# Performance work log

Measured on AMD Instinct MI355X. Metric: run time of the kernel, lower is better.

## Reference

```python
import jax, jax.numpy as jnp
import numpy as np

B = 4096          # fused tokens (batch)
E = 1024          # attnConfig embed_size == MoE emb_size
OUT = E // 4      # per-branch feature dim (self.output)
N_EXP = 8         # number of experts
TOP = 2           # top-k routing
H = 8             # attention heads
HD = E // H       # head dim
HID = 4 * E       # expert MLP hidden
IMG = 64 * 64     # flattened single-channel image
W_IMP = 0.01      # importance loss weight


def setup_inputs() -> dict:
    key = jax.random.key(0)
    ks = jax.random.split(key, 24)
    n = lambda i, shp, sc=1.0: jax.random.normal(ks[i], shp, jnp.float32) * sc
    inp = {
        'source': n(0, (B, 1, 64, 64)),
        'target': n(1, (B, 1, 64, 64)),
        'background': n(2, (B, 1, 64, 64)),
        'image': n(3, (B, E)),
        'text': n(4, (B, E)),
        # shared encoder (stub: flatten -> fc to OUT, shared across s/t/b)
        'W_enc': n(5, (IMG, OUT), 0.02), 'b_enc': jnp.zeros((OUT,), jnp.float32),
        # linerImg
        'W_img': n(6, (E, OUT), 0.02), 'b_img': jnp.zeros((OUT,), jnp.float32),
        # cross attention
        'Wq': n(7, (E, E), 0.02), 'bq': jnp.zeros((E,), jnp.float32),
        'Wk': n(8, (E, E), 0.02), 'bk': jnp.zeros((E,), jnp.float32),
        'Wv': n(9, (E, E), 0.02), 'bv': jnp.zeros((E,), jnp.float32),
        'Wo': n(10, (E, E), 0.02), 'bo': jnp.zeros((E,), jnp.float32),
        # gate
        'W_gate': n(11, (E, N_EXP), 0.02), 'b_gate': jnp.zeros((N_EXP,), jnp.float32),
        # experts: per-expert 2-layer MLP E->HID->E
        'W1': n(12, (N_EXP, E, HID), 0.02), 'b1': jnp.zeros((N_EXP, HID), jnp.float32),
        'W2': n(13, (N_EXP, HID, E), 0.02), 'b2': jnp.zeros((N_EXP, E), jnp.float32),
    }
    return inp


def reference(source, target, background, image, text,
              W_enc, b_enc, W_img, b_img,
              Wq, bq, Wk, bk, Wv, bv, Wo, bo,
              W_gate, b_gate, W1, b1, W2, b2):
    enc = lambda a: a.reshape(a.shape[0], -1) @ W_enc + b_enc      # shared_encoder stub
    s = enc(source); t = enc(target); bg = enc(background)        # [B, OUT] each
    img = jax.nn.silu(image @ W_img + b_img)                      # [B, OUT]
    x = jnp.concatenate([s, t, bg, img], axis=1)                  # [B, E] visionFeatures

    # cross attention with seq_len 1 for both x (query) and text (key/value)
    q = (x @ Wq + bq).reshape(B, H, HD)
    k = (text @ Wk + bk).reshape(B, H, HD)
    v = (text @ Wv + bv).reshape(B, H, HD)
    scores = jnp.sum(q * k, axis=-1, keepdims=True) / jnp.sqrt(jnp.float32(HD))  # [B,H,1]
    attw = jax.nn.softmax(scores[..., None], axis=-1)[..., 0]     # softmax over 1 key == 1
    att = (attw * v).reshape(B, E) @ Wo + bo                       # [B, E]

    gate_logits = att @ W_gate + b_gate                            # [B, N_EXP]
    gate_prob = jax.nn.softmax(gate_logits, axis=-1)               # eval mode: no noise
    top_w, top_idx = jax.lax.top_k(gate_prob, TOP)                 # [B, TOP]
    top_w = jax.nn.softmax(top_w, axis=-1)                         # renormalize over top-k

    # dense-dispatch equivalent of the per-expert gather/index_add loop
    h = jax.nn.gelu(jnp.einsum('be,neh->nbh', x, W1) + b1[:, None, :])   # [N,B,HID]
    y_all = jnp.einsum('nbh,nhe->nbe', h, W2) + b2[:, None, :]           # [N,B,E]
    combine = jnp.zeros((B, N_EXP), jnp.float32).at[
        jnp.arange(B)[:, None], top_idx].add(top_w)                      # [B,N]
    y = jnp.einsum('nbe,bn->be', y_all, combine)                          # [B,E]

    importance = gate_prob.sum(axis=0)                             # [N_EXP]
    importance_loss = W_IMP * (jnp.std(importance, ddof=1) / jnp.mean(importance)) ** 2
    return (y, gate_prob, importance_loss)
```

## Files before the change

### kernel.cpp

```cpp
#include <hip/hip_runtime.h>
#include <hip/hip_bf16.h>
#include <stdint.h>

typedef __bf16 bf16_t;
typedef bf16_t bf16x8 __attribute__((ext_vector_type(8)));
typedef float f32x4 __attribute__((ext_vector_type(4)));
typedef uint16_t u16x8 __attribute__((ext_vector_type(8)));

static constexpr int B_TOK  = 4096;
static constexpr int E_DIM  = 1024;
static constexpr int N_EXPC = 8;
static constexpr int HID    = 4096;
static constexpr int IMGSZ  = 4096;
static constexpr int NSLOT  = 2 * B_TOK;
static constexpr int NTIL   = 71;

#define DEVI __device__ __forceinline__

DEVI int imin(int a, int b) { return a < b ? a : b; }

DEVI uint16_t f2bf(float f) {
  union { float f; uint32_t u; } v; v.f = f;
  uint32_t u = v.u;
  return (uint16_t)((u + 0x7FFFu + ((u >> 16) & 1u)) >> 16);
}

DEVI float bf2f(uint16_t u) {
  union { uint32_t i; float f; } v; v.i = (uint32_t)u << 16; return v.f;
}

DEVI void gload_lds16(const void* g, void* l) {
  __builtin_amdgcn_global_load_lds((const __attribute__((address_space(1))) void*)g,
                                   (__attribute__((address_space(3))) void*)l, 16, 0, 0);
}

template<int N> DEVI void waitv() {
  if constexpr (N == 0)       asm volatile("s_waitcnt vmcnt(0)" ::: "memory");
  else if constexpr (N == 4)  asm volatile("s_waitcnt vmcnt(4)" ::: "memory");
  else if constexpr (N == 8)  asm volatile("s_waitcnt vmcnt(8)" ::: "memory");
  else if constexpr (N == 10) asm volatile("s_waitcnt vmcnt(10)" ::: "memory");
}

#define BAR() do { __builtin_amdgcn_sched_barrier(0); __builtin_amdgcn_s_barrier(); \
                   __builtin_amdgcn_sched_barrier(0); } while (0)

#define MFMA16(a, b, c) __builtin_amdgcn_mfma_f32_16x16x32_bf16((a), (b), (c), 0, 0, 0)

DEVI void transW_body(int bid, const float* W1, const float* W2,
                      const float* We, const float* Wi,
                      uint16_t* W1T, uint16_t* W2T, uint16_t* WeT, uint16_t* WiT,
                      float (*tile)[65])
{
  const float* in; uint16_t* out; int R, C, c0, r0;
  if (bid < 8192) {
    int e = bid >> 10, rem = bid & 1023;
    R = 1024; C = 4096;
    c0 = (rem & 63) * 64; r0 = (rem >> 6) * 64;
    in = W1 + (size_t)e * R * C; out = W1T + (size_t)e * R * C;
  } else if (bid < 16384) {
    int i = bid - 8192; int e = i >> 10, rem = i & 1023;
    R = 4096; C = 1024;
    c0 = (rem & 15) * 64; r0 = (rem >> 4) * 64;
    in = W2 + (size_t)e * R * C; out = W2T + (size_t)e * R * C;
  } else if (bid < 16640) {
    int i = bid - 16384;
    R = 4096; C = 256;
    c0 = (i & 3) * 64; r0 = (i >> 2) * 64;
    in = We; out = WeT;
  } else {
    int i = bid - 16640;
    R = 1024; C = 256;
    c0 = (i & 3) * 64; r0 = (i >> 2) * 64;
    in = Wi; out = WiT;
  }
  int t = threadIdx.x;
  #pragma unroll
  for (int i = 0; i < 4; ++i) {
    int rr = i * 16 + (t >> 4), c4 = (t & 15) * 4;
    f32x4 v = *(const f32x4*)&in[(size_t)(r0 + rr) * C + c0 + c4];
    tile[rr][c4 + 0] = v[0]; tile[rr][c4 + 1] = v[1];
    tile[rr][c4 + 2] = v[2]; tile[rr][c4 + 3] = v[3];
  }
  __syncthreads();
  #pragma unroll
  for (int i = 0; i < 2; ++i) {
    int c = i * 32 + (t >> 3), j = t & 7;
    u16x8 o;
    #pragma unroll
    for (int k = 0; k < 8; ++k) o[k] = f2bf(tile[j * 8 + k][c]);
    *(u16x8*)&out[(size_t)(c0 + c) * R + r0 + j * 8] = o;
  }
}

DEVI void matf_body(int kblk, const float* W, const float* G, float* out)
{
  int k = kblk * 4 + (threadIdx.x >> 6);
  int lane = threadIdx.x & 63;
  float a0 = 0.f, a1 = 0.f, a2 = 0.f, a3 = 0.f, a4 = 0.f, a5 = 0.f, a6 = 0.f, a7 = 0.f;
  for (int m = lane; m < E_DIM; m += 64) {
    float w = W[(size_t)k * E_DIM + m];
    const float* gm = &G[m * 8];
    a0 = __builtin_fmaf(w, gm[0], a0); a1 = __builtin_fmaf(w, gm[1], a1);
    a2 = __builtin_fmaf(w, gm[2], a2); a3 = __builtin_fmaf(w, gm[3], a3);
    a4 = __builtin_fmaf(w, gm[4], a4); a5 = __builtin_fmaf(w, gm[5], a5);
    a6 = __builtin_fmaf(w, gm[6], a6); a7 = __builtin_fmaf(w, gm[7], a7);
  }
  #pragma unroll
  for (int off = 32; off; off >>= 1) {
    a0 += __shfl_xor(a0, off); a1 += __shfl_xor(a1, off);
    a2 += __shfl_xor(a2, off); a3 += __shfl_xor(a3, off);
    a4 += __shfl_xor(a4, off); a5 += __shfl_xor(a5, off);
    a6 += __shfl_xor(a6, off); a7 += __shfl_xor(a7, off);
  }
  if (lane == 0) {
    float* o = &out[k * 8];
    o[0] = a0; o[1] = a1; o[2] = a2; o[3] = a3;
    o[4] = a4; o[5] = a5; o[6] = a6; o[7] = a7;
  }
}

__global__ __launch_bounds__(256)
void prep1_k(const float* __restrict__ W1, const float* __restrict__ W2,
             const float* __restrict__ We, const float* __restrict__ Wi,
             uint16_t* __restrict__ W1T, uint16_t* __restrict__ W2T,
             uint16_t* __restrict__ WeT, uint16_t* __restrict__ WiT,
             const float* __restrict__ Wo, const float* __restrict__ Wg,
             float* __restrict__ g1c,
             const float* __restrict__ bv, float* __restrict__ part,
             int* __restrict__ counts)
{
  __shared__ float tile[64][65];
  int bid = blockIdx.x;
  if (bid < 16704) {
    transW_body(bid, W1, W2, We, Wi, W1T, W2T, WeT, WiT, tile);
  } else if (bid < 16960) {
    matf_body(bid - 16704, Wo, Wg, g1c);
  } else if (bid < 16968) {
    int b = bid - 16960, t = threadIdx.x;
    f32x4 acc = {0.f, 0.f, 0.f, 0.f};
    for (int k = b * 128; k < b * 128 + 128; ++k) {
      float s = bv[k];
      f32x4 w = *(const f32x4*)&Wo[(size_t)k * E_DIM + t * 4];
      acc[0] = __builtin_fmaf(s, w[0], acc[0]);
      acc[1] = __builtin_fmaf(s, w[1], acc[1]);
      acc[2] = __builtin_fmaf(s, w[2], acc[2]);
      acc[3] = __builtin_fmaf(s, w[3], acc[3]);
    }
    *(f32x4*)&part[(size_t)b * E_DIM + t * 4] = acc;
  } else {
    if (threadIdx.x < 8) counts[threadIdx.x] = 0;
  }
}

__global__ __launch_bounds__(256)
void prep2_k(const float* __restrict__ Wv, const float* __restrict__ g1c,
             float* __restrict__ G3,
             const float* __restrict__ part, const float* __restrict__ bo,
             const float* __restrict__ Wg, const float* __restrict__ bg,
             float* __restrict__ gb)
{
  int bid = blockIdx.x;
  if (bid < 256) {
    matf_body(bid, Wv, g1c, G3);
  } else {
    __shared__ float t1s[E_DIM];
    int t = threadIdx.x;
    for (int j = t; j < E_DIM; j += 256) {
      float s = bo[j];
      #pragma unroll
      for (int b = 0; b < 8; ++b) s += part[(size_t)b * E_DIM + j];
      t1s[j] = s;
    }
    __syncthreads();
    int wave = t >> 6, lane = t & 63;
    #pragma unroll
    for (int ei = 0; ei < 2; ++ei) {
      int e = wave * 2 + ei;
      float s = 0.f;
      for (int m = lane; m < E_DIM; m += 64) s = __builtin_fmaf(t1s[m], Wg[m * 8 + e], s);
      #pragma unroll
      for (int off = 32; off; off >>= 1) s += __shfl_xor(s, off);
      if (lane == 0) gb[e] = s + bg[e];
    }
  }
}

__global__ __launch_bounds__(256)
void gate_k(const float* __restrict__ text, const float* __restrict__ G3,
            const float* __restrict__ gb, float* __restrict__ gate_out,
            int* __restrict__ topIdx, float* __restrict__ topW,
            int* __restrict__ counts)
{
  __shared__ __align__(16) float sT[E_DIM];
  __shared__ float lg[8];
  int b = blockIdx.x, t = threadIdx.x;
  *(f32x4*)&sT[t * 4] = *(const f32x4*)&text[(size_t)b * E_DIM + t * 4];
  __syncthreads();
  int wave = t >> 6, lane = t & 63;
  #pragma unroll
  for (int ei = 0; ei < 2; ++ei) {
    int e = wave * 2 + ei;
    float s = 0.f;
    for (int k = lane; k < E_DIM; k += 64) s = __builtin_fmaf(sT[k], G3[k * 8 + e], s);
    #pragma unroll
    for (int off = 32; off; off >>= 1) s += __shfl_down(s, off);
    if (lane == 0) lg[e] = s + gb[e];
  }
  __syncthreads();
  if (t == 0) {
    float p[8];
    float mx = lg[0];
    for (int i = 1; i < 8; i++) mx = fmaxf(mx, lg[i]);
    float den = 0.f;
    for (int i = 0; i < 8; i++) { p[i] = __expf(lg[i] - mx); den += p[i]; }
    float inv = 1.f / den;
    for (int i = 0; i < 8; i++) { p[i] *= inv; gate_out[(size_t)b * 8 + i] = p[i]; }
    int i1 = 0;
    for (int i = 1; i < 8; i++) if (p[i] > p[i1]) i1 = i;
    int i2 = (i1 == 0) ? 1 : 0;
    for (int i = 0; i < 8; i++) if (i != i1 && p[i] > p[i2]) i2 = i;
    float ex = __expf(p[i2] - p[i1]);
    float w1 = 1.f / (1.f + ex), w2 = ex / (1.f + ex);
    topIdx[b * 2] = i1; topIdx[b * 2 + 1] = i2;
    topW[b * 2] = w1;  topW[b * 2 + 1] = w2;
    atomicAdd(&counts[i1], 1);
    atomicAdd(&counts[i2], 1);
  }
}

template<int BN, int EPI, bool GATHER, int NT>
__global__ __launch_bounds__(256, 3)
void gemm_p(const uint16_t* __restrict__ Ab, int lda,
            const uint16_t* __restrict__ BT, void* __restrict__ Cv, int ldc,
            const float* __restrict__ bias, int K,
            const int* __restrict__ meta, const int* __restrict__ perm,
            size_t bStride, int biasStride)
{
  constexpr int HN = BN / 2, FN = BN / 32;
  constexpr int OPS = (BN == 128 ? 4 : 3);
  constexpr int TOTAL = NTIL * NT, Q = TOTAL / 8, FULLB = 64 * NT;
  int bid = blockIdx.x;
  int wg = (bid & 7) * Q + (bid >> 3);
  int mtile, nt;
  if (wg < FULLB) { int rem = wg % (8 * NT); mtile = (wg / (8 * NT)) * 8 + (rem & 7); nt = rem >> 3; }
  else            { int rem = wg - FULLB;    mtile = 64 + rem % 7;                    nt = rem / 7; }
  if (mtile >= meta[0]) return;
  int e = meta[1 + 3 * mtile], rowBase = meta[2 + 3 * mtile], rows = meta[3 + 3 * mtile];
  const uint16_t* Bt = BT + (size_t)e * bStride;
  const float* bi = bias + (size_t)e * (size_t)biasStride;

  constexpr int ABUF = 8192;
  constexpr int BBUF = (BN == 128) ? 8192 : 4096;
  __shared__ __align__(16) char sAraw[3 * ABUF];
  __shared__ __align__(16) char sBraw[3 * BBUF];

  int t = threadIdx.x, wave = t >> 6, lane = t & 63;
  int wr = wave >> 1, wc = wave & 1;

  int rB = t >> 2;
  int slB = ((t & 3) ^ (rB & 3)) * 8;
  const uint16_t* gB0 = Bt + (size_t)(nt * BN + rB) * K + slB;
  const uint16_t* gB1 = Bt + (size_t)(nt * BN + rB + 64) * K + slB;

  int r0 = t >> 2, r1 = r0 + 64;
  int sl = ((t & 3) ^ (r0 & 3)) * 8;
  int rr0 = imin(r0, rows - 1), rr1 = imin(r1, rows - 1);
  int car0 = GATHER ? perm[rowBase + rr0] : rowBase + rr0;
  int car1 = GATHER ? perm[rowBase + rr1] : rowBase + rr1;
  const uint16_t* gA0 = Ab + (size_t)car0 * lda + sl;
  const uint16_t* gA1 = Ab + (size_t)car1 * lda + sl;

  char* laW = sAraw + wave * 1024;
  char* lbW = sBraw + wave * 1024;
  auto STAGE = [&](int kt, int c) {
    int ko = kt << 5;
    char* la = laW + c * ABUF;
    char* lb = lbW + c * BBUF;
    gload_lds16(gA0 + ko, la);
    gload_lds16(gA1 + ko, la + 4096);
    gload_lds16(gB0 + ko, lb);
    if constexpr (BN == 128) gload_lds16(gB1 + ko, lb + 4096);
  };

  f32x4 acc[4][FN];
  #pragma unroll
  for (int m = 0; m < 4; m++)
    #pragma unroll
    for (int n = 0; n < FN; n++)
      acc[m][n] = f32x4{0.f, 0.f, 0.f, 0.f};

  STAGE(0, 0);
  STAGE(1, 1);

  int fr = lane & 15;
  int rdoff = ((lane >> 4) ^ (lane & 3)) * 16;
  int c0 = 0, c2 = 2;
  int nk = K >> 5;

  for (int kt = 0; kt < nk; ++kt) {
    if (kt + 2 < nk) { STAGE(kt + 2, c2); waitv<2 * OPS>(); }
    else if (kt + 1 < nk) waitv<OPS>();
    else waitv<0>();
    BAR();

    const char* bA = sAraw + c0 * ABUF;
    const char* bB = sBraw + c0 * BBUF;
    bf16x8 af[4], bfr[FN];
    #pragma unroll
    for (int m = 0; m < 4; m++)
      af[m] = *(const bf16x8*)(bA + (wr * 64 + m * 16 + fr) * 64 + rdoff);
    #pragma unroll
    for (int n = 0; n < FN; n++)
      bfr[n] = *(const bf16x8*)(bB + (wc * HN + n * 16 + fr) * 64 + rdoff);
    #pragma unroll
    for (int m = 0; m < 4; m++)
      #pragma unroll
      for (int n = 0; n < FN; n++)
        acc[m][n] = MFMA16(af[m], bfr[n], acc[m][n]);

    BAR();
    c0 = (c0 == 2) ? 0 : c0 + 1;
    c2 = (c2 == 2) ? 0 : c2 + 1;
  }

  #pragma unroll
  for (int m = 0; m < 4; m++) {
    int lrow = wr * 64 + m * 16 + (lane >> 4) * 4;
    #pragma unroll
    for (int n = 0; n < FN; n++) {
      int col = nt * BN + wc * HN + n * 16 + (lane & 15);
      float bval = bi[col];
      #pragma unroll
      for (int r = 0; r < 4; r++) {
        int lr = lrow + r;
        if (lr >= rows) continue;
        float v = acc[m][n][r] + bval;
        size_t cr = (size_t)(rowBase + lr) * ldc + col;
        if (EPI == 3) {
          float u = v + 0.044715f * v * v * v;
          v = v / (1.f + __expf(-1.5957691216057308f * u));
          ((uint16_t*)Cv)[cr] = f2bf(v);
        } else if (EPI == 1) {
          ((uint16_t*)Cv)[cr] = f2bf(v);
        } else {
          ((float*)Cv)[cr] = v;
        }
      }
    }
  }
}

__global__ __launch_bounds__(256, 3)
void gemm_encR(const float* __restrict__ F0, const float* __restrict__ F1,
               const float* __restrict__ F2, const float* __restrict__ Fimg,
               const uint16_t* __restrict__ BTe, const uint16_t* __restrict__ BTi,
               float* __restrict__ Penc, float* __restrict__ Pimg)
{
  int z = blockIdx.z;
  const float* Af; const uint16_t* BT; float* P; int K, Kc, k0;
  if (z < 6) {
    int br = z >> 1, kc = z & 1;
    Af = (br == 0) ? F0 : (br == 1) ? F1 : F2;
    BT = BTe; P = Penc + (size_t)z * B_TOK * 256;
    K = IMGSZ; Kc = IMGSZ / 2; k0 = kc * Kc;
  } else {
    Af = Fimg; BT = BTi; P = Pimg;
    K = E_DIM; Kc = E_DIM; k0 = 0;
  }
  int rowBase = blockIdx.x * 64, nt = blockIdx.y;

  __shared__ __align__(16) char sB[3 * 8192];
  int t = threadIdx.x, wave = t >> 6, lane = t & 63;
  int fr = lane & 15, q4 = lane >> 4;

  const float* gA = Af + (size_t)(rowBase + wave * 16 + fr) * K + k0 + q4 * 8;

  int rloc = t >> 2;
  int ssw = ((t & 3) ^ (rloc & 3)) * 8;
  const uint16_t* gB0 = BT + (size_t)(nt * 128 + rloc) * K + k0 + ssw;
  const uint16_t* gB1 = gB0 + (size_t)64 * K;

  auto STB = [&](int kt, int c) {
    gload_lds16(gB0 + kt * 32, sB + c * 8192 + wave * 1024);
    gload_lds16(gB1 + kt * 32, sB + c * 8192 + 4096 + wave * 1024);
  };

  f32x4 acc[8];
  #pragma unroll
  for (int n = 0; n < 8; ++n) acc[n] = f32x4{0.f, 0.f, 0.f, 0.f};

  int nk = Kc >> 5;
  STB(0, 0); STB(1, 1);
  f32x4 aE0 = *(const f32x4*)(gA),      aE1 = *(const f32x4*)(gA + 4);
  f32x4 aO0 = *(const f32x4*)(gA + 32), aO1 = *(const f32x4*)(gA + 36);
  int c0 = 0, c2 = 2;
  int bRow = (q4 ^ (fr & 3)) * 16;

  auto step = [&](int kt, f32x4& aX0, f32x4& aX1) {
    bool m2 = kt + 2 < nk;
    if (m2) STB(kt + 2, c2);
    bf16x8 a;
    a[0] = (bf16_t)aX0[0]; a[1] = (bf16_t)aX0[1]; a[2] = (bf16_t)aX0[2]; a[3] = (bf16_t)aX0[3];
    a[4] = (bf16_t)aX1[0]; a[5] = (bf16_t)aX1[1]; a[6] = (bf16_t)aX1[2]; a[7] = (bf16_t)aX1[3];
    int kp = m2 ? kt + 2 : kt;
    aX0 = *(const f32x4*)(gA + kp * 32);
    aX1 = *(const f32x4*)(gA + kp * 32 + 4);
    if (m2) waitv<10>(); else waitv<0>();
    BAR();
    const char* bb = sB + c0 * 8192;
    bf16x8 bfr[8];
    #pragma unroll
    for (int n = 0; n < 8; ++n)
      bfr[n] = *(const bf16x8*)(bb + n * 1024 + fr * 64 + bRow);
    #pragma unroll
    for (int n = 0; n < 8; ++n) acc[n] = MFMA16(a, bfr[n], acc[n]);
    BAR();
    c0 = (c0 == 2) ? 0 : c0 + 1;
    c2 = (c2 == 2) ? 0 : c2 + 1;
  };

  for (int kt = 0; kt < nk; kt += 2) {
    step(kt, aE0, aE1);
    step(kt + 1, aO0, aO1);
  }

  #pragma unroll
  for (int n = 0; n < 8; ++n) {
    int col = nt * 128 + n * 16 + fr;
    #pragma unroll
    for (int r = 0; r < 4; ++r) {
      int row = rowBase + wave * 16 + q4 * 4 + r;
      P[(size_t)row * 256 + col] = acc[n][r];
    }
  }
}

__global__ __launch_bounds__(256)
void redupost_k(const float* __restrict__ Penc, const float* __restrict__ Pimg,
                const float* __restrict__ bEnc, const float* __restrict__ bImg,
                uint16_t* __restrict__ xb,
                const float* __restrict__ gate_out, float* __restrict__ out_loss,
                const int* __restrict__ counts, const int* __restrict__ topIdx,
                const float* __restrict__ topW,
                int* __restrict__ meta, int* __restrict__ perm,
                int* __restrict__ slotOf)
{
  int y = blockIdx.y, t = threadIdx.x;
  if (y < 4) {
    int row = blockIdx.x * 4 + (t >> 6);
    int c4 = (t & 63) * 4;
    bool img = (y == 3);
    const float* bias = img ? bImg : bEnc;
    f32x4 s = *(const f32x4*)&bias[c4];
    if (img) {
      s += *(const f32x4*)&Pimg[(size_t)row * 256 + c4];
      #pragma unroll
      for (int j = 0; j < 4; ++j) s[j] = s[j] / (1.f + __expf(-s[j]));
    } else {
      const float* p = Penc + (size_t)y * 2 * B_TOK * 256 + (size_t)row * 256 + c4;
      s += *(const f32x4*)p;
      s += *(const f32x4*)(p + (size_t)B_TOK * 256);
    }
    ushort4 o;
    o.x = f2bf(s[0]); o.y = f2bf(s[1]); o.z = f2bf(s[2]); o.w = f2bf(s[3]);
    *(ushort4*)&xb[(size_t)row * E_DIM + y * 256 + c4] = o;
    return;
  }
  if (blockIdx.x == 0) {
    float s[8] = {0.f, 0.f, 0.f, 0.f, 0.f, 0.f, 0.f, 0.f};
    for (int b = t; b < B_TOK; b += 256) {
      const float* g = &gate_out[(size_t)b * 8];
      #pragma unroll
      for (int e = 0; e < 8; ++e) s[e] += g[e];
    }
    __shared__ float red[8][256];
    #pragma unroll
    for (int e = 0; e < 8; ++e) red[e][t] = s[e];
    __syncthreads();
    for (int off = 128; off; off >>= 1) {
      if (t < off)
        #pragma unroll
        for (int e = 0; e < 8; ++e) red[e][t] += red[e][t + off];
      __syncthreads();
    }
    if (t == 0) {
      float m = 0.f;
      for (int e = 0; e < 8; e++) m += red[e][0];
      m *= 0.125f;
      float v = 0.f;
      for (int e = 0; e < 8; e++) { float d = red[e][0] - m; v += d * d; }
      v /= 7.f;
      out_loss[0] = 0.01f * v / (m * m);
    }
  } else if (blockIdx.x == 1) {
    __shared__ int sBases[8];
    __shared__ int sCursor[8];
    if (t == 0) {
      int a = 0, nt = 0;
      for (int e = 0; e < 8; e++) {
        sBases[e] = a; sCursor[e] = 0;
        int c = counts[e];
        for (int j = 0; j < c; j += 128) {
          meta[1 + 3 * nt] = e;
          meta[2 + 3 * nt] = a + j;
          meta[3 + 3 * nt] = (c - j < 128) ? (c - j) : 128;
          nt++;
        }
        a += c;
      }
      meta[0] = nt;
    }
    __syncthreads();
    for (int b = t; b < B_TOK; b += 256) {
      #pragma unroll
      for (int j = 0; j < 2; j++) {
        int e = topIdx[b * 2 + j];
        int pos = atomicAdd(&sCursor[e], 1);
        int slot = sBases[e] + pos;
        perm[slot] = b;
        slotOf[b * 2 + j] = slot;
      }
    }
  }
}

__global__ __launch_bounds__(256)
void combine_k(const uint16_t* __restrict__ Yg, const int* __restrict__ slotOf,
               const float* __restrict__ topW, float* __restrict__ y)
{
  int b = blockIdx.x, t = threadIdx.x;
  int s0 = slotOf[b * 2], s1 = slotOf[b * 2 + 1];
  float w0 = topW[b * 2], w1 = topW[b * 2 + 1];
  ushort4 ua = *(const ushort4*)&Yg[(size_t)s0 * E_DIM + t * 4];
  ushort4 uc = *(const ushort4*)&Yg[(size_t)s1 * E_DIM + t * 4];
  f32x4 r;
  r[0] = bf2f(ua.x) * w0 + bf2f(uc.x) * w1;
  r[1] = bf2f(ua.y) * w0 + bf2f(uc.y) * w1;
  r[2] = bf2f(ua.z) * w0 + bf2f(uc.z) * w1;
  r[3] = bf2f(ua.w) * w0 + bf2f(uc.w) * w1;
  *(f32x4*)&y[(size_t)b * E_DIM + t * 4] = r;
}

extern "C" void kernel_launch(void* const* d_in, const int* in_sizes, int n_in,
                              void* d_out, int out_size, void* d_ws, size_t ws_size,
                              hipStream_t stream)
{
  (void)in_sizes; (void)n_in; (void)out_size;
  const float* src   = (const float*)d_in[0];
  const float* tgt   = (const float*)d_in[1];
  const float* bgr   = (const float*)d_in[2];
  const float* image = (const float*)d_in[3];
  const float* text  = (const float*)d_in[4];
  const float* W_enc = (const float*)d_in[5];
  const float* b_enc = (const float*)d_in[6];
  const float* W_img = (const float*)d_in[7];
  const float* b_img = (const float*)d_in[8];
  const float* Wv    = (const float*)d_in[13];
  const float* bv    = (const float*)d_in[14];
  const float* Wo    = (const float*)d_in[15];
  const float* bo    = (const float*)d_in[16];
  const float* Wg    = (const float*)d_in[17];
  const float* bgg   = (const float*)d_in[18];
  const float* W1    = (const float*)d_in[19];
  const float* b1    = (const float*)d_in[20];
  const float* W2    = (const float*)d_in[21];
  const float* b2    = (const float*)d_in[22];

  float* out_y    = (float*)d_out;
  float* out_gate = out_y + (size_t)B_TOK * E_DIM;
  float* out_loss = out_gate + (size_t)B_TOK * N_EXPC;

  char* p = (char*)d_ws;
  auto alloc = [&](size_t bytes) { char* r = p; p += (bytes + 255) & ~(size_t)255; return r; };
  uint16_t* WencT = (uint16_t*)alloc((size_t)256 * IMGSZ * 2);
  uint16_t* WimgT = (uint16_t*)alloc((size_t)256 * E_DIM * 2);
  uint16_t* W1T   = (uint16_t*)alloc((size_t)N_EXPC * HID * E_DIM * 2);
  uint16_t* W2T   = (uint16_t*)alloc((size_t)N_EXPC * E_DIM * HID * 2);
  float* part  = (float*)alloc((size_t)8 * E_DIM * 4);
  float* g1c   = (float*)alloc((size_t)E_DIM * 8 * 4);
  float* G3    = (float*)alloc((size_t)E_DIM * 8 * 4);
  float* gbv   = (float*)alloc(64 * 4);
  int*   topIdx = (int*)alloc(B_TOK * 2 * 4);
  float* topW   = (float*)alloc(B_TOK * 2 * 4);
  int*   slotOf = (int*)alloc(B_TOK * 2 * 4);
  int*   counts = (int*)alloc(64 * 4);
  int*   meta   = (int*)alloc((1 + 3 * (NTIL + 1)) * 4 + 64);
  int*   perm   = (int*)alloc(NSLOT * 4);
  uint16_t* xbf  = (uint16_t*)alloc((size_t)B_TOK * E_DIM * 2);
  uint16_t* Hbuf = (uint16_t*)alloc((size_t)NSLOT * HID * 2);
  char* uni = alloc((size_t)7 * B_TOK * 256 * 4);
  float* Penc = (float*)uni;
  float* Pimg = Penc + (size_t)6 * B_TOK * 256;
  uint16_t* Yg = (uint16_t*)uni;
  if ((size_t)(p - (char*)d_ws) > ws_size) return;

  prep1_k<<<dim3(16969), 256, 0, stream>>>(W1, W2, W_enc, W_img, W1T, W2T, WencT, WimgT,
                                           Wo, Wg, g1c, bv, part, counts);
  prep2_k<<<dim3(257), 256, 0, stream>>>(Wv, g1c, G3, part, bo, Wg, bgg, gbv);
  gate_k<<<B_TOK, 256, 0, stream>>>(text, G3, gbv, out_gate, topIdx, topW, counts);
  gemm_encR<<<dim3(B_TOK / 64, 2, 7), 256, 0, stream>>>(
      src, tgt, bgr, image, WencT, WimgT, Penc, Pimg);
  redupost_k<<<dim3(B_TOK / 4, 5), 256, 0, stream>>>(
      Penc, Pimg, b_enc, b_img, xbf,
      out_gate, out_loss, counts, topIdx, topW, meta, perm, slotOf);

  gemm_p<128, 3, true, HID / 128><<<dim3(NTIL * (HID / 128)), 256, 0, stream>>>(
      xbf, E_DIM, W1T, Hbuf, HID, b1, E_DIM, meta, perm, (size_t)HID * E_DIM, HID);
  gemm_p<128, 1, false, E_DIM / 128><<<dim3(NTIL * (E_DIM / 128)), 256, 0, stream>>>(
      Hbuf, HID, W2T, Yg, E_DIM, b2, HID, meta, perm, (size_t)E_DIM * HID, E_DIM);

  combine_k<<<B_TOK, 256, 0, stream>>>(Yg, slotOf, topW, out_y);
}
```

Baseline: 633.9 us.

## Deepen GEMM K-step to 64 with double buffering and 8-way LDS swizzle

The grouped expert GEMM kernel now stages 64-wide K slices instead of 32-wide, using two LDS buffers of 16 KB each for A and B instead of a triple-buffered 32-wide ring. The LDS swizzle changes from 4-way to an 8-way XOR pattern over 128-byte rows. Each iteration issues twice as many MFMAs per barrier pair, which halves the barrier and wait overhead per unit of work. In exchange the pipeline is only one stage ahead, and the larger LDS footprint lowers occupancy (launch bounds drop from 3 to 2 blocks per CU).

```diff
diff --git a/kernel.cpp b/kernel.cpp
--- a/kernel.cpp
+++ b/kernel.cpp
@@ -36,7 +36,6 @@
 
 template<int N> DEVI void waitv() {
   if constexpr (N == 0)       asm volatile("s_waitcnt vmcnt(0)" ::: "memory");
-  else if constexpr (N == 4)  asm volatile("s_waitcnt vmcnt(4)" ::: "memory");
   else if constexpr (N == 8)  asm volatile("s_waitcnt vmcnt(8)" ::: "memory");
   else if constexpr (N == 10) asm volatile("s_waitcnt vmcnt(10)" ::: "memory");
 }
@@ -228,16 +227,14 @@
   }
 }
 
-template<int BN, int EPI, bool GATHER, int NT>
-__global__ __launch_bounds__(256, 3)
-void gemm_p(const uint16_t* __restrict__ Ab, int lda,
-            const uint16_t* __restrict__ BT, void* __restrict__ Cv, int ldc,
-            const float* __restrict__ bias, int K,
-            const int* __restrict__ meta, const int* __restrict__ perm,
-            size_t bStride, int biasStride)
-{
-  constexpr int HN = BN / 2, FN = BN / 32;
-  constexpr int OPS = (BN == 128 ? 4 : 3);
+template<int EPI, bool GATHER, int NT>
+__global__ __launch_bounds__(256, 2)
+void gemm_p64(const uint16_t* __restrict__ Ab, int lda,
+              const uint16_t* __restrict__ BT, void* __restrict__ Cv, int ldc,
+              const float* __restrict__ bias, int K,
+              const int* __restrict__ meta, const int* __restrict__ perm,
+              size_t bStride, int biasStride)
+{
   constexpr int TOTAL = NTIL * NT, Q = TOTAL / 8, FULLB = 64 * NT;
   int bid = blockIdx.x;
   int wg = (bid & 7) * Q + (bid >> 3);
@@ -249,86 +246,86 @@
   const uint16_t* Bt = BT + (size_t)e * bStride;
   const float* bi = bias + (size_t)e * (size_t)biasStride;
 
-  constexpr int ABUF = 8192;
-  constexpr int BBUF = (BN == 128) ? 8192 : 4096;
-  __shared__ __align__(16) char sAraw[3 * ABUF];
-  __shared__ __align__(16) char sBraw[3 * BBUF];
+  __shared__ __align__(16) char sA[2 * 16384];
+  __shared__ __align__(16) char sB[2 * 16384];
 
   int t = threadIdx.x, wave = t >> 6, lane = t & 63;
   int wr = wave >> 1, wc = wave & 1;
 
-  int rB = t >> 2;
-  int slB = ((t & 3) ^ (rB & 3)) * 8;
-  const uint16_t* gB0 = Bt + (size_t)(nt * BN + rB) * K + slB;
-  const uint16_t* gB1 = Bt + (size_t)(nt * BN + rB + 64) * K + slB;
-
-  int r0 = t >> 2, r1 = r0 + 64;
-  int sl = ((t & 3) ^ (r0 & 3)) * 8;
-  int rr0 = imin(r0, rows - 1), rr1 = imin(r1, rows - 1);
-  int car0 = GATHER ? perm[rowBase + rr0] : rowBase + rr0;
-  int car1 = GATHER ? perm[rowBase + rr1] : rowBase + rr1;
-  const uint16_t* gA0 = Ab + (size_t)car0 * lda + sl;
-  const uint16_t* gA1 = Ab + (size_t)car1 * lda + sl;
-
-  char* laW = sAraw + wave * 1024;
-  char* lbW = sBraw + wave * 1024;
+  int r8 = t >> 3;
+  int sg = (((t & 7) ^ (r8 & 7))) * 8;
+  const uint16_t* gA[4];
+  const uint16_t* gB[4];
+  #pragma unroll
+  for (int i = 0; i < 4; ++i) {
+    int ar = imin(i * 32 + r8, rows - 1);
+    int car = GATHER ? perm[rowBase + ar] : rowBase + ar;
+    gA[i] = Ab + (size_t)car * lda + sg;
+    gB[i] = Bt + (size_t)(nt * 128 + i * 32 + r8) * K + sg;
+  }
+  int wO = wave * 1024;
+
   auto STAGE = [&](int kt, int c) {
-    int ko = kt << 5;
-    char* la = laW + c * ABUF;
-    char* lb = lbW + c * BBUF;
-    gload_lds16(gA0 + ko, la);
-    gload_lds16(gA1 + ko, la + 4096);
-    gload_lds16(gB0 + ko, lb);
-    if constexpr (BN == 128) gload_lds16(gB1 + ko, lb + 4096);
+    int ko = kt << 6;
+    char* la = sA + c * 16384 + wO;
+    char* lb = sB + c * 16384 + wO;
+    #pragma unroll
+    for (int i = 0; i < 4; ++i) gload_lds16(gA[i] + ko, la + i * 4096);
+    #pragma unroll
+    for (int i = 0; i < 4; ++i) gload_lds16(gB[i] + ko, lb + i * 4096);
   };
 
-  f32x4 acc[4][FN];
+  f32x4 acc[4][4];
   #pragma unroll
   for (int m = 0; m < 4; m++)
     #pragma unroll
-    for (int n = 0; n < FN; n++)
+    for (int n = 0; n < 4; n++)
       acc[m][n] = f32x4{0.f, 0.f, 0.f, 0.f};
 
   STAGE(0, 0);
-  STAGE(1, 1);
-
-  int fr = lane & 15;
-  int rdoff = ((lane >> 4) ^ (lane & 3)) * 16;
-  int c0 = 0, c2 = 2;
-  int nk = K >> 5;
+
+  int fr = lane & 15, q4 = lane >> 4;
+  int nk = K >> 6;
 
   for (int kt = 0; kt < nk; ++kt) {
-    if (kt + 2 < nk) { STAGE(kt + 2, c2); waitv<2 * OPS>(); }
-    else if (kt + 1 < nk) waitv<OPS>();
+    int b = kt & 1, nb = b ^ 1;
+    bool more = kt + 1 < nk;
+    if (more) { STAGE(kt + 1, nb); waitv<8>(); }
     else waitv<0>();
     BAR();
 
-    const char* bA = sAraw + c0 * ABUF;
-    const char* bB = sBraw + c0 * BBUF;
-    bf16x8 af[4], bfr[FN];
-    #pragma unroll
-    for (int m = 0; m < 4; m++)
-      af[m] = *(const bf16x8*)(bA + (wr * 64 + m * 16 + fr) * 64 + rdoff);
-    #pragma unroll
-    for (int n = 0; n < FN; n++)
-      bfr[n] = *(const bf16x8*)(bB + (wc * HN + n * 16 + fr) * 64 + rdoff);
-    #pragma unroll
-    for (int m = 0; m < 4; m++)
-      #pragma unroll
-      for (int n = 0; n < FN; n++)
-        acc[m][n] = MFMA16(af[m], bfr[n], acc[m][n]);
-
+    const char* bA = sA + b * 16384;
+    const char* bB = sB + b * 16384;
+    #pragma unroll
+    for (int ks = 0; ks < 2; ++ks) {
+      bf16x8 af[4], bfr[4];
+      #pragma unroll
+      for (int m = 0; m < 4; m++) {
+        int rr = wr * 64 + m * 16 + fr;
+        int sidx = (ks * 4 + q4) ^ (rr & 7);
+        af[m] = *(const bf16x8*)(bA + rr * 128 + sidx * 16);
+      }
+      #pragma unroll
+      for (int n = 0; n < 4; n++) {
+        int rr = wc * 64 + n * 16 + fr;
+        int sidx = (ks * 4 + q4) ^ (rr & 7);
+        bfr[n] = *(const bf16x8*)(bB + rr * 128 + sidx * 16);
+      }
+      #pragma unroll
+      for (int m = 0; m < 4; m++)
+        #pragma unroll
+        for (int n = 0; n < 4; n++)
+          acc[m][n] = MFMA16(af[m], bfr[n], acc[m][n]);
+    }
     BAR();
-    c0 = (c0 == 2) ? 0 : c0 + 1;
-    c2 = (c2 == 2) ? 0 : c2 + 1;
   }
 
   #pragma unroll
   for (int m = 0; m < 4; m++) {
-    int lrow = wr * 64 + m * 16 + (lane >> 4) * 4;
-    #pragma unroll
-    for (int n = 0; n < FN; n++) {
-      int col = nt * BN + wc * HN + n * 16 + (lane & 15);
+    int lrow = wr * 64 + m * 16 + q4 * 4;
+    #pragma unroll
+    for (int n = 0; n < 4; n++) {
+      int col = nt * 128 + wc * 64 + n * 16 + fr;
       float bval = bi[col];
       #pragma unroll
       for (int r = 0; r < 4; r++) {
@@ -340,10 +337,8 @@
           float u = v + 0.044715f * v * v * v;
           v = v / (1.f + __expf(-1.5957691216057308f * u));
           ((uint16_t*)Cv)[cr] = f2bf(v);
-        } else if (EPI == 1) {
+        } else {
           ((uint16_t*)Cv)[cr] = f2bf(v);
-        } else {
-          ((float*)Cv)[cr] = v;
         }
       }
     }
@@ -604,9 +599,9 @@
       Penc, Pimg, b_enc, b_img, xbf,
       out_gate, out_loss, counts, topIdx, topW, meta, perm, slotOf);
 
-  gemm_p<128, 3, true, HID / 128><<<dim3(NTIL * (HID / 128)), 256, 0, stream>>>(
+  gemm_p64<3, true, HID / 128><<<dim3(NTIL * (HID / 128)), 256, 0, stream>>>(
       xbf, E_DIM, W1T, Hbuf, HID, b1, E_DIM, meta, perm, (size_t)HID * E_DIM, HID);
-  gemm_p<128, 1, false, E_DIM / 128><<<dim3(NTIL * (E_DIM / 128)), 256, 0, stream>>>(
+  gemm_p64<1, false, E_DIM / 128><<<dim3(NTIL * (E_DIM / 128)), 256, 0, stream>>>(
       Hbuf, HID, W2T, Yg, E_DIM, b2, HID, meta, perm, (size_t)E_DIM * HID, E_DIM);
 
   combine_k<<<B_TOK, 256, 0, stream>>>(Yg, slotOf, topW, out_y);
```

Measured after the change: 698.6 us. +10.2%, slower.
